# Kernel tuning notes

Hardware: AMD Instinct MI355X
Metric: run time of the kernel (lower is better)

Reference implementation:

```python
import jax, jax.numpy as jnp
import numpy as np

B, LQ, LK = 4, 2048, 2048
XS, YS, PD = 1024, 1024, 128


def setup_inputs() -> dict:
    key = jax.random.key(0)
    ks = jax.random.split(key, 8)
    s_x = 1.0 / np.sqrt(XS)
    s_y = 1.0 / np.sqrt(YS)
    return {
        "x": jax.random.normal(ks[0], (B, LQ, XS), dtype=jnp.float32),
        "y": jax.random.normal(ks[1], (B, LK, YS), dtype=jnp.float32),
        "Wq": jax.random.normal(ks[2], (XS, PD), dtype=jnp.float32) * s_x,
        "bq": jax.random.normal(ks[3], (PD,), dtype=jnp.float32) * 0.01,
        "Wk": jax.random.normal(ks[4], (YS, PD), dtype=jnp.float32) * s_y,
        "bk": jax.random.normal(ks[5], (PD,), dtype=jnp.float32) * 0.01,
        "Wv": jax.random.normal(ks[6], (YS, PD), dtype=jnp.float32) * s_y,
        "bv": jax.random.normal(ks[7], (PD,), dtype=jnp.float32) * 0.01,
        "mask": 1,
    }


def reference(x, y, Wq, bq, Wk, bk, Wv, bv, mask):
    # Projections (torch Linear: x @ W^T + b; here weights stored as [in, out])
    q = x @ Wq + bq  # [B, LQ, PD]
    k = y @ Wk + bk  # [B, LK, PD]
    v = y @ Wv + bv  # [B, LK, PD]
    scale = 1.0 / jnp.sqrt(jnp.asarray(PD, dtype=q.dtype))
    att = jax.nn.softmax(jnp.einsum("bqd,bkd->bqk", q, k) * scale, axis=-1)
    if mask:
        # NOTE: faithful to original — triu applied AFTER softmax (diagonal=1),
        # zeroing the lower triangle + diagonal without renormalizing.
        att = jnp.triu(att, k=1)
    return jnp.einsum("bqk,bkd->bqd", att, v)  # [B, LQ, PD]
```

## Files before the change

### kernel.cpp

```cpp
#include <hip/hip_runtime.h>

typedef short s8v __attribute__((ext_vector_type(8)));
typedef float f4v __attribute__((ext_vector_type(4)));

#define NB 4
#define LQ 2048
#define LKK 2048
#define XS 1024
#define PDD 128

#define PST 68
#define AST 132

__device__ __forceinline__ ushort f2bf(float x) {
  union { float f; uint u; } v; v.f = x;
  uint r = (v.u + 0x7fffu + ((v.u >> 16) & 1u)) >> 16;
  return (ushort)r;
}


__global__ __launch_bounds__(256) void k_wtrans(const float* __restrict__ Wq,
                                                const float* __restrict__ Wk,
                                                const float* __restrict__ Wv,
                                                ushort* __restrict__ Wt) {
  int p = blockIdx.y;
  const float* W = (p == 0) ? Wq : (p == 1) ? Wk : Wv;
  ushort* out = Wt + (size_t)p * (PDD * XS);
  int t = threadIdx.x;
  int n = t >> 1;
  int kk0 = (t & 1) * 16;
  int k0 = blockIdx.x * 32;
  ushort tmp[16];
#pragma unroll
  for (int i = 0; i < 16; ++i) tmp[i] = f2bf(W[(size_t)(k0 + kk0 + i) * PDD + n]);
  uint4 u0, u1;
  u0.x = tmp[0] | ((uint)tmp[1] << 16);  u0.y = tmp[2] | ((uint)tmp[3] << 16);
  u0.z = tmp[4] | ((uint)tmp[5] << 16);  u0.w = tmp[6] | ((uint)tmp[7] << 16);
  u1.x = tmp[8] | ((uint)tmp[9] << 16);  u1.y = tmp[10] | ((uint)tmp[11] << 16);
  u1.z = tmp[12] | ((uint)tmp[13] << 16); u1.w = tmp[14] | ((uint)tmp[15] << 16);
  uint4* dst = (uint4*)&out[n * XS + k0 + kk0];
  dst[0] = u0; dst[1] = u1;
}

__global__ __launch_bounds__(256, 3) void k_proj(const float* __restrict__ x,
                                                 const float* __restrict__ y,
                                                 const ushort* __restrict__ Wt,
                                                 const float* __restrict__ bq,
                                                 const float* __restrict__ bk,
                                                 const float* __restrict__ bv,
                                                 ushort* __restrict__ qo,
                                                 ushort* __restrict__ ko,
                                                 ushort* __restrict__ vt) {
  int bx = blockIdx.x;
  int p = bx >> 8;
  int tile = bx & 255;
  const float* in = (p == 0) ? x : y;
  const ushort* wt = Wt + (size_t)p * (PDD * XS);
  int row0 = tile * 32;
  __shared__ ushort As[32 * 72];
  __shared__ ushort Bs[128 * 72];
  int t = threadIdx.x, wave = t >> 6, lane = t & 63, quad = lane >> 4, lc = lane & 15;

  int ar = t >> 3, ac0 = (t & 7) * 8;
  int bn = t >> 1, bk0 = (t & 1) * 32;
  const float* asrc = in + (size_t)(row0 + ar) * XS + ac0;
  const ushort* bsrc = wt + (size_t)bn * XS + bk0;

  float4 ra0, ra1;
  uint4 rb0, rb1, rb2, rb3;
  auto load = [&](int k0) {
    const float* ap = asrc + k0;
    ra0 = *(const float4*)ap;
    ra1 = *(const float4*)(ap + 4);
    const ushort* bp = bsrc + k0;
    rb0 = *(const uint4*)bp;
    rb1 = *(const uint4*)(bp + 8);
    rb2 = *(const uint4*)(bp + 16);
    rb3 = *(const uint4*)(bp + 24);
  };
  auto store = [&]() {
    uint4 pa;
    pa.x = f2bf(ra0.x) | ((uint)f2bf(ra0.y) << 16);
    pa.y = f2bf(ra0.z) | ((uint)f2bf(ra0.w) << 16);
    pa.z = f2bf(ra1.x) | ((uint)f2bf(ra1.y) << 16);
    pa.w = f2bf(ra1.z) | ((uint)f2bf(ra1.w) << 16);
    *(uint4*)&As[ar * 72 + ac0] = pa;
    *(uint4*)&Bs[bn * 72 + bk0] = rb0;
    *(uint4*)&Bs[bn * 72 + bk0 + 8] = rb1;
    *(uint4*)&Bs[bn * 72 + bk0 + 16] = rb2;
    *(uint4*)&Bs[bn * 72 + bk0 + 24] = rb3;
  };

  const f4v z4 = {0.f, 0.f, 0.f, 0.f};
  f4v acc[2][2];
#pragma unroll
  for (int m = 0; m < 2; ++m)
#pragma unroll
    for (int n = 0; n < 2; ++n) acc[m][n] = z4;

  load(0);
#pragma unroll 1
  for (int k0 = 0; k0 < XS; k0 += 64) {
    store();
    __syncthreads();
    load((k0 + 64) & (XS - 1));
#pragma unroll
    for (int kc = 0; kc < 2; ++kc) {
      s8v a0 = *(const s8v*)&As[lc * 72 + kc * 32 + quad * 8];
      s8v a1 = *(const s8v*)&As[(16 + lc) * 72 + kc * 32 + quad * 8];
      s8v b0 = *(const s8v*)&Bs[(wave * 32 + lc) * 72 + kc * 32 + quad * 8];
      s8v b1 = *(const s8v*)&Bs[(wave * 32 + 16 + lc) * 72 + kc * 32 + quad * 8];
      acc[0][0] = __builtin_amdgcn_mfma_f32_16x16x32_bf16(a0, b0, acc[0][0], 0, 0, 0);
      acc[0][1] = __builtin_amdgcn_mfma_f32_16x16x32_bf16(a0, b1, acc[0][1], 0, 0, 0);
      acc[1][0] = __builtin_amdgcn_mfma_f32_16x16x32_bf16(a1, b0, acc[1][0], 0, 0, 0);
      acc[1][1] = __builtin_amdgcn_mfma_f32_16x16x32_bf16(a1, b1, acc[1][1], 0, 0, 0);
    }
    __syncthreads();
  }

  const float qscale = 0.08838834764831845f;
  const float* bias = (p == 0) ? bq : (p == 1) ? bk : bv;
  if (p < 2) {
    ushort* o = (p == 0) ? qo : ko;
    float scl = (p == 0) ? qscale : 1.0f;
    int bb2 = row0 >> 11;
    int rloc = row0 & 2047;
#pragma unroll
    for (int m = 0; m < 2; ++m) {
      int qt = (rloc >> 4) + m;
#pragma unroll
      for (int n = 0; n < 2; ++n) {
        int col = wave * 32 + n * 16 + lc;
        float bb = bias[col];
        size_t base = ((((size_t)(bb2 * 128 + qt) * 4 + wave) * 4 + (n * 2 + (lc >> 3))) * 16 +
                       quad * 4) * 8 + (lc & 7);
#pragma unroll
        for (int g = 0; g < 4; ++g)
          o[base + (size_t)g * 8] = f2bf((acc[m][n][g] + bb) * scl);
      }
    }
  } else {
#pragma unroll
    for (int m = 0; m < 2; ++m) {
      int rbase = row0 + m * 16 + quad * 4;
      int bb2 = rbase >> 11, rr = rbase & 2047;
      int kchunk = rr >> 5, qv = (rr >> 3) & 3, jj0 = rr & 7;
#pragma unroll
      for (int n = 0; n < 2; ++n) {
        int col = wave * 32 + n * 16 + lc;
        int dt = wave * 2 + n;
        float bb = bias[col];
        ushort4 pk;
        pk.x = f2bf(acc[m][n][0] + bb);
        pk.y = f2bf(acc[m][n][1] + bb);
        pk.z = f2bf(acc[m][n][2] + bb);
        pk.w = f2bf(acc[m][n][3] + bb);
        size_t off = ((((size_t)(bb2 * 64 + kchunk) * 8 + dt) * 4 + qv) * 16 + lc) * 8 + jj0;
        *(ushort4*)&vt[off] = pk;
      }
    }
  }
}

__global__ __launch_bounds__(512, 2) void k_attn(const ushort* __restrict__ qg,
                                                 const ushort* __restrict__ kg,
                                                 const ushort* __restrict__ vtg,
                                                 const int* __restrict__ maskp,
                                                 float* __restrict__ out) {
  __shared__ float smem[8 * 32 * PST];
  __shared__ float lS[8][2][16];
  int bx = blockIdx.x;
  int xcd = bx & 7;
  int b = xcd >> 1;
  int q0 = ((bx >> 3) * 2 + (xcd & 1)) * 32;
  int t = threadIdx.x;
  int wave = t >> 6, lane = t & 63, quad = lane >> 4, lc = lane & 15;
  int domask = *maskp;
  float* Psw = smem + wave * (32 * PST);

  const ushort* qB = qg + ((size_t)(b * 128 + (q0 >> 4))) * 2048 + lane * 8;
  s8v aq[2][4];
#pragma unroll
  for (int m = 0; m < 2; ++m)
#pragma unroll
    for (int kc = 0; kc < 4; ++kc)
      aq[m][kc] = *(const s8v*)(qB + m * 2048 + kc * 512);

  const f4v z4 = {0.f, 0.f, 0.f, 0.f};
  f4v acc[2][8];
#pragma unroll
  for (int m = 0; m < 2; ++m)
#pragma unroll
    for (int i = 0; i < 8; ++i) acc[m][i] = z4;
  float rs[2][4] = {{0.f, 0.f, 0.f, 0.f}, {0.f, 0.f, 0.f, 0.f}};

#pragma unroll 1
  for (int i = 0; i < 4; ++i) {
    int kt = wave + i * 8;

    const ushort* kB = kg + ((size_t)(b * 128 + i * 32 + wave * 4)) * 2048 + lane * 8;
    s8v kf[16];
#pragma unroll
    for (int f = 0; f < 16; ++f) kf[f] = *(const s8v*)(kB + f * 512);

    f4v sf[2][4];
#pragma unroll
    for (int nt = 0; nt < 4; ++nt) {
      f4v s0 = z4, s1 = z4;
#pragma unroll
      for (int kc = 0; kc < 4; ++kc) {
        s0 = __builtin_amdgcn_mfma_f32_16x16x32_bf16(aq[0][kc], kf[nt * 4 + kc], s0, 0, 0, 0);
        s1 = __builtin_amdgcn_mfma_f32_16x16x32_bf16(aq[1][kc], kf[nt * 4 + kc], s1, 0, 0, 0);
      }
      sf[0][nt] = s0;
      sf[1][nt] = s1;
    }

    const ushort* vB = vtg + ((size_t)(b * 64 + i * 16 + wave * 2)) * 4096 + lane * 8;
    s8v vf[16];
#pragma unroll
    for (int f = 0; f < 16; ++f) vf[f] = *(const s8v*)(vB + f * 512);
    __builtin_amdgcn_sched_barrier(0);

#pragma unroll
    for (int m = 0; m < 2; ++m)
#pragma unroll
      for (int g = 0; g < 4; ++g) {
        int rg = q0 + m * 16 + quad * 4 + g;
#pragma unroll
        for (int nt = 0; nt < 4; ++nt) {
          float pv = __expf(sf[m][nt][g]);
          rs[m][g] += pv;
          int jg = kt * 64 + nt * 16 + lc;
          if (domask && (jg <= rg)) pv = 0.f;
          Psw[(m * 16 + quad * 4 + g) * PST + nt * 16 + lc] = pv;
        }
      }

#pragma unroll
    for (int jc = 0; jc < 2; ++jc)
#pragma unroll
      for (int m = 0; m < 2; ++m) {
        const float* pp = &Psw[(m * 16 + lc) * PST + jc * 32 + quad * 8];
        float4 p0 = *(const float4*)pp;
        float4 p1 = *(const float4*)(pp + 4);
        s8v ap;
        ap[0] = (short)f2bf(p0.x); ap[1] = (short)f2bf(p0.y);
        ap[2] = (short)f2bf(p0.z); ap[3] = (short)f2bf(p0.w);
        ap[4] = (short)f2bf(p1.x); ap[5] = (short)f2bf(p1.y);
        ap[6] = (short)f2bf(p1.z); ap[7] = (short)f2bf(p1.w);
#pragma unroll
        for (int dt = 0; dt < 8; ++dt) {
          acc[m][dt] = __builtin_amdgcn_mfma_f32_16x16x32_bf16(ap, vf[jc * 8 + dt], acc[m][dt], 0, 0, 0);
        }
      }
  }

#pragma unroll
  for (int off = 8; off >= 1; off >>= 1)
#pragma unroll
    for (int m = 0; m < 2; ++m)
#pragma unroll
      for (int g = 0; g < 4; ++g) rs[m][g] += __shfl_xor(rs[m][g], off, 64);

  __syncthreads();
  if (lc == 0) {
#pragma unroll
    for (int m = 0; m < 2; ++m)
#pragma unroll
      for (int g = 0; g < 4; ++g) lS[wave][m][quad * 4 + g] = rs[m][g];
  }

#pragma unroll
  for (int m = 0; m < 2; ++m) {
#pragma unroll
    for (int dt = 0; dt < 8; ++dt)
#pragma unroll
      for (int g = 0; g < 4; ++g)
        smem[wave * (16 * AST) + (quad * 4 + g) * AST + dt * 16 + lc] = acc[m][dt][g];
    __syncthreads();
    {
      int row = t >> 5, c0 = (t & 31) * 4;
      float L = 0.f;
      float ox = 0.f, oy = 0.f, oz = 0.f, ow = 0.f;
#pragma unroll
      for (int p = 0; p < 8; ++p) {
        L += lS[p][m][row];
        const float* a = &smem[p * (16 * AST) + row * AST + c0];
        float4 xv = *(const float4*)a;
        ox += xv.x; oy += xv.y; oz += xv.z; ow += xv.w;
      }
      float inv = 1.0f / L;
      float4 o;
      o.x = ox * inv; o.y = oy * inv; o.z = oz * inv; o.w = ow * inv;
      float* op = out + ((size_t)(b * LQ + q0 + m * 16 + row)) * PDD + c0;
      *(float4*)op = o;
    }
    __syncthreads();
  }
}

extern "C" void kernel_launch(void* const* d_in, const int* in_sizes, int n_in,
                              void* d_out, int out_size, void* d_ws, size_t ws_size,
                              hipStream_t stream) {
  const float* x  = (const float*)d_in[0];
  const float* y  = (const float*)d_in[1];
  const float* Wq = (const float*)d_in[2];
  const float* bq = (const float*)d_in[3];
  const float* Wk = (const float*)d_in[4];
  const float* bk = (const float*)d_in[5];
  const float* Wv = (const float*)d_in[6];
  const float* bv = (const float*)d_in[7];
  const int* mask = (const int*)d_in[8];
  char* ws = (char*)d_ws;
  ushort* qb = (ushort*)(ws);
  ushort* kb = (ushort*)(ws + (size_t)(1 << 21));
  ushort* vt = (ushort*)(ws + (size_t)(2 << 21));
  ushort* Wt = (ushort*)(ws + (size_t)(3 << 21));
  float* out = (float*)d_out;

  hipLaunchKernelGGL(k_wtrans, dim3(32, 3), dim3(256), 0, stream, Wq, Wk, Wv, Wt);
  hipLaunchKernelGGL(k_proj, dim3(768), dim3(256), 0, stream, x, y, Wt, bq, bk, bv, qb, kb, vt);
  hipLaunchKernelGGL(k_attn, dim3(256), dim3(512), 0, stream, qb, kb, vt, mask, out);
}
```

Baseline: 142.1 us.

## Fuse K and V projections and stage whole A rows in LDS

```diff
diff --git a/kernel.cpp b/kernel.cpp
--- a/kernel.cpp
+++ b/kernel.cpp
@@ -38,11 +38,13 @@
   u0.z = tmp[4] | ((uint)tmp[5] << 16);  u0.w = tmp[6] | ((uint)tmp[7] << 16);
   u1.x = tmp[8] | ((uint)tmp[9] << 16);  u1.y = tmp[10] | ((uint)tmp[11] << 16);
   u1.z = tmp[12] | ((uint)tmp[13] << 16); u1.w = tmp[14] | ((uint)tmp[15] << 16);
-  uint4* dst = (uint4*)&out[n * XS + k0 + kk0];
-  dst[0] = u0; dst[1] = u1;
-}
-
-__global__ __launch_bounds__(256, 3) void k_proj(const float* __restrict__ x,
+  int ct = n >> 4, lc = n & 15, kq = k0 >> 5;
+  ushort* base = out + ((size_t)(ct * 32 + kq)) * 512 + (kk0 >> 3) * 128 + lc * 8;
+  *(uint4*)base = u0;
+  *(uint4*)(base + 128) = u1;
+}
+
+__global__ __launch_bounds__(256, 2) void k_proj(const float* __restrict__ x,
                                                  const float* __restrict__ y,
                                                  const ushort* __restrict__ Wt,
                                                  const float* __restrict__ bq,
@@ -51,111 +53,121 @@
                                                  ushort* __restrict__ qo,
                                                  ushort* __restrict__ ko,
                                                  ushort* __restrict__ vt) {
+  __shared__ ushort As[32 * 1032];
   int bx = blockIdx.x;
-  int p = bx >> 8;
-  int tile = bx & 255;
-  const float* in = (p == 0) ? x : y;
-  const ushort* wt = Wt + (size_t)p * (PDD * XS);
-  int row0 = tile * 32;
-  __shared__ ushort As[32 * 72];
-  __shared__ ushort Bs[128 * 72];
+  int xcd = bx & 7;
+  int b = xcd >> 1;
+  int half = xcd & 1;
+  int idx = bx >> 3;
+  int kind = idx & 1;
+  int rt = (idx >> 1) + half * 32;
+  int row0 = b * 2048 + rt * 32;
+  const float* in = kind ? y : x;
   int t = threadIdx.x, wave = t >> 6, lane = t & 63, quad = lane >> 4, lc = lane & 15;
 
-  int ar = t >> 3, ac0 = (t & 7) * 8;
-  int bn = t >> 1, bk0 = (t & 1) * 32;
-  const float* asrc = in + (size_t)(row0 + ar) * XS + ac0;
-  const ushort* bsrc = wt + (size_t)bn * XS + bk0;
-
-  float4 ra0, ra1;
-  uint4 rb0, rb1, rb2, rb3;
-  auto load = [&](int k0) {
-    const float* ap = asrc + k0;
-    ra0 = *(const float4*)ap;
-    ra1 = *(const float4*)(ap + 4);
-    const ushort* bp = bsrc + k0;
-    rb0 = *(const uint4*)bp;
-    rb1 = *(const uint4*)(bp + 8);
-    rb2 = *(const uint4*)(bp + 16);
-    rb3 = *(const uint4*)(bp + 24);
-  };
-  auto store = [&]() {
-    uint4 pa;
-    pa.x = f2bf(ra0.x) | ((uint)f2bf(ra0.y) << 16);
-    pa.y = f2bf(ra0.z) | ((uint)f2bf(ra0.w) << 16);
-    pa.z = f2bf(ra1.x) | ((uint)f2bf(ra1.y) << 16);
-    pa.w = f2bf(ra1.z) | ((uint)f2bf(ra1.w) << 16);
-    *(uint4*)&As[ar * 72 + ac0] = pa;
-    *(uint4*)&Bs[bn * 72 + bk0] = rb0;
-    *(uint4*)&Bs[bn * 72 + bk0 + 8] = rb1;
-    *(uint4*)&Bs[bn * 72 + bk0 + 16] = rb2;
-    *(uint4*)&Bs[bn * 72 + bk0 + 24] = rb3;
-  };
+  {
+    int r = t >> 3, c0 = (t & 7) * 128;
+    const float* src = in + (size_t)(row0 + r) * XS + c0;
+    ushort* dst = &As[r * 1032 + c0];
+#pragma unroll
+    for (int s = 0; s < 8; ++s) {
+      float4 f0 = *(const float4*)(src + s * 16);
+      float4 f1 = *(const float4*)(src + s * 16 + 4);
+      float4 f2 = *(const float4*)(src + s * 16 + 8);
+      float4 f3 = *(const float4*)(src + s * 16 + 12);
+      uint4 p0, p1;
+      p0.x = f2bf(f0.x) | ((uint)f2bf(f0.y) << 16);
+      p0.y = f2bf(f0.z) | ((uint)f2bf(f0.w) << 16);
+      p0.z = f2bf(f1.x) | ((uint)f2bf(f1.y) << 16);
+      p0.w = f2bf(f1.z) | ((uint)f2bf(f1.w) << 16);
+      p1.x = f2bf(f2.x) | ((uint)f2bf(f2.y) << 16);
+      p1.y = f2bf(f2.z) | ((uint)f2bf(f2.w) << 16);
+      p1.z = f2bf(f3.x) | ((uint)f2bf(f3.y) << 16);
+      p1.w = f2bf(f3.z) | ((uint)f2bf(f3.w) << 16);
+      *(uint4*)(dst + s * 16) = p0;
+      *(uint4*)(dst + s * 16 + 8) = p1;
+    }
+  }
+  __syncthreads();
 
   const f4v z4 = {0.f, 0.f, 0.f, 0.f};
-  f4v acc[2][2];
+  f4v acc0[2][2], acc1[2][2];
 #pragma unroll
   for (int m = 0; m < 2; ++m)
 #pragma unroll
-    for (int n = 0; n < 2; ++n) acc[m][n] = z4;
-
-  load(0);
-#pragma unroll 1
-  for (int k0 = 0; k0 < XS; k0 += 64) {
-    store();
-    __syncthreads();
-    load((k0 + 64) & (XS - 1));
-#pragma unroll
-    for (int kc = 0; kc < 2; ++kc) {
-      s8v a0 = *(const s8v*)&As[lc * 72 + kc * 32 + quad * 8];
-      s8v a1 = *(const s8v*)&As[(16 + lc) * 72 + kc * 32 + quad * 8];
-      s8v b0 = *(const s8v*)&Bs[(wave * 32 + lc) * 72 + kc * 32 + quad * 8];
-      s8v b1 = *(const s8v*)&Bs[(wave * 32 + 16 + lc) * 72 + kc * 32 + quad * 8];
-      acc[0][0] = __builtin_amdgcn_mfma_f32_16x16x32_bf16(a0, b0, acc[0][0], 0, 0, 0);
-      acc[0][1] = __builtin_amdgcn_mfma_f32_16x16x32_bf16(a0, b1, acc[0][1], 0, 0, 0);
-      acc[1][0] = __builtin_amdgcn_mfma_f32_16x16x32_bf16(a1, b0, acc[1][0], 0, 0, 0);
-      acc[1][1] = __builtin_amdgcn_mfma_f32_16x16x32_bf16(a1, b1, acc[1][1], 0, 0, 0);
-    }
-    __syncthreads();
+    for (int n = 0; n < 2; ++n) { acc0[m][n] = z4; acc1[m][n] = z4; }
+
+  const ushort* w0 = Wt + (size_t)(kind ? 1 : 0) * (PDD * XS) + lane * 8;
+  const ushort* w1 = Wt + (size_t)2 * (PDD * XS) + lane * 8;
+  int ct0 = wave * 2;
+
+#pragma unroll 4
+  for (int kq = 0; kq < 32; ++kq) {
+    s8v a0 = *(const s8v*)&As[lc * 1032 + kq * 32 + quad * 8];
+    s8v a1 = *(const s8v*)&As[(16 + lc) * 1032 + kq * 32 + quad * 8];
+    s8v b00 = *(const s8v*)(w0 + ((size_t)(ct0 * 32 + kq)) * 512);
+    s8v b01 = *(const s8v*)(w0 + ((size_t)((ct0 + 1) * 32 + kq)) * 512);
+    acc0[0][0] = __builtin_amdgcn_mfma_f32_16x16x32_bf16(a0, b00, acc0[0][0], 0, 0, 0);
+    acc0[0][1] = __builtin_amdgcn_mfma_f32_16x16x32_bf16(a0, b01, acc0[0][1], 0, 0, 0);
+    acc0[1][0] = __builtin_amdgcn_mfma_f32_16x16x32_bf16(a1, b00, acc0[1][0], 0, 0, 0);
+    acc0[1][1] = __builtin_amdgcn_mfma_f32_16x16x32_bf16(a1, b01, acc0[1][1], 0, 0, 0);
+    if (kind) {
+      s8v b10 = *(const s8v*)(w1 + ((size_t)(ct0 * 32 + kq)) * 512);
+      s8v b11 = *(const s8v*)(w1 + ((size_t)((ct0 + 1) * 32 + kq)) * 512);
+      acc1[0][0] = __builtin_amdgcn_mfma_f32_16x16x32_bf16(a0, b10, acc1[0][0], 0, 0, 0);
+      acc1[0][1] = __builtin_amdgcn_mfma_f32_16x16x32_bf16(a0, b11, acc1[0][1], 0, 0, 0);
+      acc1[1][0] = __builtin_amdgcn_mfma_f32_16x16x32_bf16(a1, b10, acc1[1][0], 0, 0, 0);
+      acc1[1][1] = __builtin_amdgcn_mfma_f32_16x16x32_bf16(a1, b11, acc1[1][1], 0, 0, 0);
+    }
   }
 
   const float qscale = 0.08838834764831845f;
-  const float* bias = (p == 0) ? bq : (p == 1) ? bk : bv;
-  if (p < 2) {
-    ushort* o = (p == 0) ? qo : ko;
-    float scl = (p == 0) ? qscale : 1.0f;
-    int bb2 = row0 >> 11;
-    int rloc = row0 & 2047;
+  int rloc = rt * 32;
+  if (kind == 0) {
 #pragma unroll
     for (int m = 0; m < 2; ++m) {
       int qt = (rloc >> 4) + m;
 #pragma unroll
       for (int n = 0; n < 2; ++n) {
         int col = wave * 32 + n * 16 + lc;
-        float bb = bias[col];
-        size_t base = ((((size_t)(bb2 * 128 + qt) * 4 + wave) * 4 + (n * 2 + (lc >> 3))) * 16 +
+        float bb = bq[col];
+        size_t base = ((((size_t)(b * 128 + qt) * 4 + wave) * 4 + (n * 2 + (lc >> 3))) * 16 +
                        quad * 4) * 8 + (lc & 7);
 #pragma unroll
         for (int g = 0; g < 4; ++g)
-          o[base + (size_t)g * 8] = f2bf((acc[m][n][g] + bb) * scl);
+          qo[base + (size_t)g * 8] = f2bf((acc0[m][n][g] + bb) * qscale);
       }
     }
   } else {
 #pragma unroll
     for (int m = 0; m < 2; ++m) {
-      int rbase = row0 + m * 16 + quad * 4;
-      int bb2 = rbase >> 11, rr = rbase & 2047;
+      int qt = (rloc >> 4) + m;
+#pragma unroll
+      for (int n = 0; n < 2; ++n) {
+        int col = wave * 32 + n * 16 + lc;
+        float bb = bk[col];
+        size_t base = ((((size_t)(b * 128 + qt) * 4 + wave) * 4 + (n * 2 + (lc >> 3))) * 16 +
+                       quad * 4) * 8 + (lc & 7);
+#pragma unroll
+        for (int g = 0; g < 4; ++g)
+          ko[base + (size_t)g * 8] = f2bf(acc0[m][n][g] + bb);
+      }
+    }
+#pragma unroll
+    for (int m = 0; m < 2; ++m) {
+      int rr = rloc + m * 16 + quad * 4;
       int kchunk = rr >> 5, qv = (rr >> 3) & 3, jj0 = rr & 7;
 #pragma unroll
       for (int n = 0; n < 2; ++n) {
         int col = wave * 32 + n * 16 + lc;
         int dt = wave * 2 + n;
-        float bb = bias[col];
+        float bb = bv[col];
         ushort4 pk;
-        pk.x = f2bf(acc[m][n][0] + bb);
-        pk.y = f2bf(acc[m][n][1] + bb);
-        pk.z = f2bf(acc[m][n][2] + bb);
-        pk.w = f2bf(acc[m][n][3] + bb);
-        size_t off = ((((size_t)(bb2 * 64 + kchunk) * 8 + dt) * 4 + qv) * 16 + lc) * 8 + jj0;
+        pk.x = f2bf(acc1[m][n][0] + bb);
+        pk.y = f2bf(acc1[m][n][1] + bb);
+        pk.z = f2bf(acc1[m][n][2] + bb);
+        pk.w = f2bf(acc1[m][n][3] + bb);
+        size_t off = ((((size_t)(b * 64 + kchunk) * 8 + dt) * 4 + qv) * 16 + lc) * 8 + jj0;
         *(ushort4*)&vt[off] = pk;
       }
     }
@@ -320,6 +332,6 @@
   float* out = (float*)d_out;
 
   hipLaunchKernelGGL(k_wtrans, dim3(32, 3), dim3(256), 0, stream, Wq, Wk, Wv, Wt);
-  hipLaunchKernelGGL(k_proj, dim3(768), dim3(256), 0, stream, x, y, Wt, bq, bk, bv, qb, kb, vt);
+  hipLaunchKernelGGL(k_proj, dim3(512), dim3(256), 0, stream, x, y, Wt, bq, bk, bv, qb, kb, vt);
   hipLaunchKernelGGL(k_attn, dim3(256), dim3(512), 0, stream, qb, kb, vt, mask, out);
 }
```

After: 145.9 us. +2.7%, slower.
